# Kernel optimization log

Hardware: AMD Instinct MI355X
Metric: run time of the kernel (lower is better)

Reference implementation:

```python
import jax, jax.numpy as jnp
import numpy as np

B, S, E, H = 4, 2048, 2048, 16
D = E // H  # 128


def _rope(x, sin, cos):
    # x: (B, S, H, D); sin/cos: (S, D//2)
    x1, x2 = jnp.split(x, 2, axis=-1)
    c = cos[None, :, None, :]
    s = sin[None, :, None, :]
    return jnp.concatenate([x1 * c - x2 * s, x1 * s + x2 * c], axis=-1)


def setup_inputs() -> dict:
    key = jax.random.key(0)
    ks = jax.random.split(key, 12)
    inp = {
        "x_q": jax.random.normal(ks[0], (B, S, E), jnp.float32),
        "x_kv": jax.random.normal(ks[1], (B, S, E), jnp.float32),
        "Wq": jax.random.normal(ks[2], (E, E), jnp.float32) / np.sqrt(E),
        "bq": jnp.zeros((E,), jnp.float32),
        "Wk": jax.random.normal(ks[3], (E, E), jnp.float32) / np.sqrt(E),
        "bk": jnp.zeros((E,), jnp.float32),
        "Wv": jax.random.normal(ks[4], (E, E), jnp.float32) / np.sqrt(E),
        "bv": jnp.zeros((E,), jnp.float32),
        "Wo": jax.random.normal(ks[5], (E, E), jnp.float32) / np.sqrt(E),
        "bo": jnp.zeros((E,), jnp.float32),
        "angles": jax.random.uniform(ks[6], (2, S, D // 2), jnp.float32),
        "attn_mask": jnp.ones((B, S), jnp.int32),
        "causal": 0,
        "k_rope": 1,
    }
    return inp


def reference(x_q, x_kv, Wq, bq, Wk, bk, Wv, bv, Wo, bo, angles, attn_mask, causal, k_rope):
    sin, cos = angles[0], angles[1]
    q = (x_q @ Wq.T + bq).reshape(B, S, H, D)
    k = (x_kv @ Wk.T + bk).reshape(B, S, H, D)
    v = (x_kv @ Wv.T + bv).reshape(B, S, H, D)
    q = _rope(q, sin, cos)
    if k_rope:
        k = _rope(k, sin, cos)
    # scaled dot-product attention, heads leading: (B, H, S, S)
    scores = jnp.einsum("bqhd,bkhd->bhqk", q, k) / np.sqrt(D).astype(np.float32)
    mask = attn_mask.astype(bool)[:, None, None, :]  # (B,1,1,S_kv)
    if causal:
        cm = jnp.tril(jnp.ones((S, S), bool))[None, None]
        mask = mask & cm
    scores = jnp.where(mask, scores, jnp.finfo(scores.dtype).min)
    probs = jax.nn.softmax(scores, axis=-1)
    attn = jnp.einsum("bhqk,bkhd->bqhd", probs, v).reshape(B, S, E)
    return attn @ Wo.T + bo
```

## Files before the change

### kernel.cpp

```cpp
#include <hip/hip_runtime.h>
#include <hip/hip_bf16.h>


typedef __bf16 bf16;
typedef __bf16 bf16x8 __attribute__((ext_vector_type(8)));
typedef __bf16 bf16x4 __attribute__((ext_vector_type(4)));
typedef __bf16 bf16x2 __attribute__((ext_vector_type(2)));
typedef float  f32x4  __attribute__((ext_vector_type(4)));
typedef float  f32x16 __attribute__((ext_vector_type(16)));

constexpr int Bc = 4, Sc = 2048, Ec = 2048, Hc = 16, Dc = 128;
constexpr int Mc = Bc * Sc;

__device__ __forceinline__ void async16(const void* g, void* l) {
  __builtin_amdgcn_global_load_lds(
      (const __attribute__((address_space(1))) void*)g,
      (__attribute__((address_space(3))) void*)l, 16, 0, 0);
}

__device__ __forceinline__ unsigned int pkbf(float a, float b) {
  union { bf16x2 v; unsigned int u; } c;
  c.v[0] = (bf16)a; c.v[1] = (bf16)b;
  return c.u;
}

__device__ __forceinline__ int swzb32(int r, int kb) {
  int b = r * 64 + kb;
  return b ^ (((b >> 9) & 1) << 5);
}

__global__ void cvt_multi(const float* s0, const float* s1, const float* s2, const float* s3,
                          bf16* d0, bf16* d1, bf16* d2, bf16* d3, int n8) {
  const float* src; bf16* dst;
  switch (blockIdx.y) {
    case 0:  src = s0; dst = d0; break;
    case 1:  src = s1; dst = d1; break;
    case 2:  src = s2; dst = d2; break;
    default: src = s3; dst = d3; break;
  }
  int i = blockIdx.x * blockDim.x + threadIdx.x;
  const int stride = gridDim.x * blockDim.x;
  for (; i < n8; i += stride) {
    const float4 a = *((const float4*)src + (size_t)i * 2);
    const float4 b = *((const float4*)src + (size_t)i * 2 + 1);
    bf16x8 o;
    o[0] = (bf16)a.x; o[1] = (bf16)a.y; o[2] = (bf16)a.z; o[3] = (bf16)a.w;
    o[4] = (bf16)b.x; o[5] = (bf16)b.y; o[6] = (bf16)b.z; o[7] = (bf16)b.w;
    *(bf16x8*)(dst + (size_t)i * 8) = o;
  }
}

template <int OUT>
__global__ __launch_bounds__(512, 2) void gemm8(
    const bf16* __restrict__ A, const bf16* __restrict__ Bm,
    const float* __restrict__ bias, void* __restrict__ Cout, int Mblocks)
{
  __shared__ __align__(16) bf16 lds[4 * 16384];
  const int tid = threadIdx.x;
  const int w = tid >> 6, lane = tid & 63;
  const int l15 = lane & 15, l16 = lane >> 4;
  const int wm = w >> 2, wn = w & 3;
  const int id = blockIdx.x;
  const int nwg = Mblocks * 8, cpx = nwg >> 3;
  const int swz = (id & 7) * cpx + (id >> 3);
  const int by = swz >> 3, bx = swz & 7;
  const long m0 = (long)by * 256, n0 = (long)bx * 256;
  constexpr int NT = 64;

  auto stA = [&](int buf, long kt, int j) {
    int c = w * 128 + j * 64 + lane;
    int cs = c ^ (((c >> 5) & 1) << 1);
    async16(A + (m0 + (cs >> 2)) * 2048 + kt + (cs & 3) * 8,
            &lds[buf * 16384 + c * 8]);
  };
  auto stB = [&](int buf, long kt, int j) {
    int c = w * 128 + j * 64 + lane;
    int cs = c ^ (((c >> 5) & 1) << 1);
    async16(Bm + (n0 + (cs >> 2)) * 2048 + kt + (cs & 3) * 8,
            &lds[buf * 16384 + 8192 + c * 8]);
  };

  f32x4 acc[8][4];
#pragma unroll
  for (int a = 0; a < 8; ++a)
#pragma unroll
    for (int b = 0; b < 4; ++b) acc[a][b] = f32x4{0.f, 0.f, 0.f, 0.f};

  stA(0, 0, 0);  stA(0, 0, 1);  stB(0, 0, 0);  stB(0, 0, 1);
  stA(1, 32, 0); stA(1, 32, 1); stB(1, 32, 0); stB(1, 32, 1);
  stA(2, 64, 0); stA(2, 64, 1); stB(2, 64, 0); stB(2, 64, 1);
  asm volatile("s_waitcnt vmcnt(8)" ::: "memory");
  __builtin_amdgcn_s_barrier();

  int cur = 0, nx = 3;
  for (int t = 0; t < NT; ++t) {
    const char* Ab = (const char*)&lds[cur * 16384];
    const char* Bb = Ab + 16384;
    const long ktn = (long)(t + 3) * 32;
    const bool pf = (t < NT - 3);

    bf16x8 af[8], bf0[2];
#pragma unroll
    for (int mf = 0; mf < 8; ++mf)
      af[mf] = *(const bf16x8*)(Ab + swzb32(wm * 128 + mf * 16 + l15, l16 * 16));
#pragma unroll
    for (int nf = 0; nf < 2; ++nf)
      bf0[nf] = *(const bf16x8*)(Bb + swzb32(wn * 64 + nf * 16 + l15, l16 * 16));
    if (pf) { stA(nx, ktn, 0); stA(nx, ktn, 1); }
    asm volatile("" ::: "memory");
    __builtin_amdgcn_s_barrier();
    __builtin_amdgcn_s_setprio(1);
#pragma unroll
    for (int mf = 0; mf < 8; ++mf)
#pragma unroll
      for (int nf = 0; nf < 2; ++nf)
        acc[mf][nf] = __builtin_amdgcn_mfma_f32_16x16x32_bf16(af[mf], bf0[nf], acc[mf][nf], 0, 0, 0);
    __builtin_amdgcn_s_setprio(0);
    __builtin_amdgcn_s_barrier();

    bf16x8 bf1[2];
#pragma unroll
    for (int nf = 0; nf < 2; ++nf)
      bf1[nf] = *(const bf16x8*)(Bb + swzb32(wn * 64 + (2 + nf) * 16 + l15, l16 * 16));
    if (pf) { stB(nx, ktn, 0); stB(nx, ktn, 1); }
    asm volatile("" ::: "memory");
    __builtin_amdgcn_s_barrier();
    __builtin_amdgcn_s_setprio(1);
#pragma unroll
    for (int mf = 0; mf < 8; ++mf)
#pragma unroll
      for (int nf = 0; nf < 2; ++nf)
        acc[mf][2 + nf] = __builtin_amdgcn_mfma_f32_16x16x32_bf16(af[mf], bf1[nf], acc[mf][2 + nf], 0, 0, 0);
    __builtin_amdgcn_s_setprio(0);
    if (t < NT - 3)       { asm volatile("s_waitcnt vmcnt(8)" ::: "memory"); }
    else if (t == NT - 3) { asm volatile("s_waitcnt vmcnt(4)" ::: "memory"); }
    else if (t == NT - 2) { asm volatile("s_waitcnt vmcnt(0)" ::: "memory"); }
    __builtin_amdgcn_s_barrier();
    cur = (cur + 1) & 3;
    nx  = (nx + 1) & 3;
  }

#pragma unroll
  for (int mf = 0; mf < 8; ++mf)
#pragma unroll
    for (int nf = 0; nf < 4; ++nf) {
      const long m = m0 + wm * 128 + mf * 16 + l16 * 4;
      const long n = n0 + wn * 64 + nf * 16 + l15;
      const float bv = bias[n];
      if (OUT == 2) {
        const long bb = m >> 11, ss = m & 2047;
        const long head = n >> 7, d = n & 127;
        bf16x4 st;
#pragma unroll
        for (int i = 0; i < 4; ++i) st[i] = (bf16)(acc[mf][nf][i] + bv);
        *(bf16x4*)((bf16*)Cout + ((((bb << 4) + head) << 7) + d) * 2048 + ss) = st;
      } else {
#pragma unroll
        for (int i = 0; i < 4; ++i) {
          float v = acc[mf][nf][i] + bv;
          if (OUT == 1) ((bf16*)Cout)[(m + i) * 2048 + n] = (bf16)v;
          else          ((float*)Cout)[(m + i) * 2048 + n] = v;
        }
      }
    }
}

__global__ void rope_kernel(bf16* __restrict__ x, const float* __restrict__ angles,
                            const int* __restrict__ flag, int force)
{
  if (!force && flag[0] == 0) return;
  const int t = threadIdx.x;
  const long R = (long)blockIdx.x * 64 + (t >> 2);
  const int d0 = (t & 3) * 16;
  const long s = (R / Hc) % Sc;
  bf16* rowp = x + R * Dc;
  bf16x8 lo0 = *(bf16x8*)(rowp + d0);
  bf16x8 lo1 = *(bf16x8*)(rowp + d0 + 8);
  bf16x8 hi0 = *(bf16x8*)(rowp + d0 + 64);
  bf16x8 hi1 = *(bf16x8*)(rowp + d0 + 72);
  const float* sp = angles + s * 64 + d0;
  const float* cp = angles + 131072 + s * 64 + d0;
  bf16x8 a0, a1, b0, b1;
#pragma unroll
  for (int j = 0; j < 8; ++j) {
    float c = cp[j], sn = sp[j];
    float x1 = (float)lo0[j], x2 = (float)hi0[j];
    a0[j] = (bf16)(x1 * c - x2 * sn);
    b0[j] = (bf16)(x1 * sn + x2 * c);
    float c1 = cp[j + 8], sn1 = sp[j + 8];
    float y1 = (float)lo1[j], y2 = (float)hi1[j];
    a1[j] = (bf16)(y1 * c1 - y2 * sn1);
    b1[j] = (bf16)(y1 * sn1 + y2 * c1);
  }
  *(bf16x8*)(rowp + d0)      = a0;
  *(bf16x8*)(rowp + d0 + 8)  = a1;
  *(bf16x8*)(rowp + d0 + 64) = b0;
  *(bf16x8*)(rowp + d0 + 72) = b1;
}

__global__ __launch_bounds__(256, 2) void attn_kernel(
    const bf16* __restrict__ q0, const bf16* __restrict__ k0,
    const bf16* __restrict__ vt, const int* __restrict__ mask,
    const int* __restrict__ causal_p, const float* __restrict__ angles,
    bf16* __restrict__ attn_out)
{
  __shared__ __align__(16) bf16 Ks[2][64 * 128];
  __shared__ __align__(16) bf16 Vs[128 * 64];

  const int tid = threadIdx.x, wid = tid >> 6, lane = tid & 63;
  const int l31 = lane & 31, h = lane >> 5;
  const int id = blockIdx.x;
  const int swz = (id & 7) * 128 + (id >> 3);
  const int bh = swz >> 4, qb = swz & 15;
  const int b = bh >> 4, hh = bh & 15;
  const int q_glob = qb * 128 + wid * 32 + l31;
  const int causal_f = causal_p[0];
  const float SC = 0.08838834764831845f * 1.4426950408889634f;
  const float NEG = -3.0e38f;

  auto stageK = [&](int kv0s, int bufs) {
#pragma unroll
    for (int it = 0; it < 4; ++it) {
      int g = it * 256 + tid;
      int r = g >> 4, gp = g & 15;
      async16(k0 + ((size_t)(b * Sc + kv0s + r) * Hc + hh) * Dc + ((gp ^ (r & 15)) << 3),
              &Ks[bufs][g * 8]);
    }
  };
  auto stageV = [&](int kv0s) {
#pragma unroll
    for (int it = 0; it < 4; ++it) {
      int g = it * 256 + tid;
      int r = g >> 3, gp = g & 7;
      async16(vt + ((size_t)bh * Dc + r) * Sc + kv0s + ((gp ^ (r & 7)) << 3),
              &Vs[g * 8]);
    }
  };

  bf16x8 qf[8];
  {
    const bf16* qrow = q0 + ((size_t)(b * Sc + q_glob) * Hc + hh) * Dc;
#pragma unroll
    for (int dc = 0; dc < 4; ++dc) {
      bf16x8 lo = *(const bf16x8*)(qrow + dc * 16 + h * 8);
      bf16x8 hi = *(const bf16x8*)(qrow + (dc + 4) * 16 + h * 8);
      const float* sp = angles + (size_t)q_glob * 64 + dc * 16 + h * 8;
      union { float4 v[2]; float f[8]; } sn, cs;
      sn.v[0] = ((const float4*)sp)[0];
      sn.v[1] = ((const float4*)sp)[1];
      cs.v[0] = ((const float4*)(sp + 131072))[0];
      cs.v[1] = ((const float4*)(sp + 131072))[1];
#pragma unroll
      for (int j = 0; j < 8; ++j) {
        float x1 = (float)lo[j], x2 = (float)hi[j];
        qf[dc][j]     = (bf16)(SC * (x1 * cs.f[j] - x2 * sn.f[j]));
        qf[dc + 4][j] = (bf16)(SC * (x1 * sn.f[j] + x2 * cs.f[j]));
      }
    }
  }

  f32x16 o[4];
#pragma unroll
  for (int db = 0; db < 4; ++db)
#pragma unroll
    for (int r = 0; r < 16; ++r) o[db][r] = 0.f;
  float mrun = NEG, lrun = 0.f;

  stageK(0, 0);
  const int mv0 = mask[b * Sc + lane];
  asm volatile("s_waitcnt vmcnt(0)" ::: "memory");
  __builtin_amdgcn_s_barrier();
  unsigned long long mbits = __ballot(mv0 != 0);
  int cur = 0;

  for (int kv0 = 0; kv0 < Sc; kv0 += 64) {
    const int kvn = kv0 + 64;
    const bool has_next = (kvn < Sc);
    unsigned long long mbits_next = ~0ull;
    if (has_next) {
      const int mvn = mask[b * Sc + kvn + lane];
      mbits_next = __ballot(mvn != 0);
    }
    stageV(kv0);
    if (has_next) stageK(kvn, cur ^ 1);

    f32x16 s;
#pragma unroll
    for (int r = 0; r < 16; ++r) s[r] = 0.f;
    __builtin_amdgcn_s_setprio(1);
#pragma unroll
    for (int dc = 0; dc < 8; ++dc) {
      bf16x8 kf = *(const bf16x8*)&Ks[cur][l31 * 128 + (((dc * 2 + h) ^ (l31 & 15)) << 3)];
      s = __builtin_amdgcn_mfma_f32_32x32x16_bf16(kf, qf[dc], s, 0, 0, 0);
    }
    __builtin_amdgcn_s_setprio(0);
    if (mbits != ~0ull) {
#pragma unroll
      for (int r = 0; r < 16; ++r) {
        int off = (r & 3) + 8 * (r >> 2) + 4 * h;
        if (!((mbits >> off) & 1)) s[r] = NEG;
      }
    }
    if (causal_f) {
#pragma unroll
      for (int r = 0; r < 16; ++r) {
        int kvg = kv0 + (r & 3) + 8 * (r >> 2) + 4 * h;
        if (kvg > q_glob) s[r] = NEG;
      }
    }
    {
      float tmax = s[0];
#pragma unroll
      for (int r = 1; r < 16; ++r) tmax = fmaxf(tmax, s[r]);
      tmax = fmaxf(tmax, __shfl_xor(tmax, 32));
      if (!__all(tmax <= mrun + 8.0f)) {
        const float mnew = fmaxf(mrun, tmax);
        const float alpha = __builtin_amdgcn_exp2f(mrun - mnew);
#pragma unroll
        for (int db = 0; db < 4; ++db)
#pragma unroll
          for (int r = 0; r < 16; ++r) o[db][r] *= alpha;
        lrun *= alpha;
        mrun = mnew;
      }
      float rs = 0.f;
#pragma unroll
      for (int r = 0; r < 16; ++r) {
        s[r] = __builtin_amdgcn_exp2f(s[r] - mrun);
        rs += s[r];
      }
      rs += __shfl_xor(rs, 32);
      lrun += rs;
    }
    unsigned int dw0 = pkbf(s[0], s[1]),   dw1 = pkbf(s[2], s[3]);
    unsigned int dw2 = pkbf(s[4], s[5]),   dw3 = pkbf(s[6], s[7]);
    unsigned int dw4 = pkbf(s[8], s[9]),   dw5 = pkbf(s[10], s[11]);
    unsigned int dw6 = pkbf(s[12], s[13]), dw7 = pkbf(s[14], s[15]);
    asm volatile("v_permlane32_swap_b32 %0, %1" : "+v"(dw0), "+v"(dw2));
    asm volatile("v_permlane32_swap_b32 %0, %1" : "+v"(dw1), "+v"(dw3));
    asm volatile("v_permlane32_swap_b32 %0, %1" : "+v"(dw4), "+v"(dw6));
    asm volatile("v_permlane32_swap_b32 %0, %1" : "+v"(dw5), "+v"(dw7));
    union { unsigned int u[4]; bf16x8 v; } pf0, pf1;
    pf0.u[0] = dw0; pf0.u[1] = dw1; pf0.u[2] = dw2; pf0.u[3] = dw3;
    pf1.u[0] = dw4; pf1.u[1] = dw5; pf1.u[2] = dw6; pf1.u[3] = dw7;

    if (has_next) { asm volatile("s_waitcnt vmcnt(4)" ::: "memory"); }
    else          { asm volatile("s_waitcnt vmcnt(0)" ::: "memory"); }
    __builtin_amdgcn_s_barrier();

    __builtin_amdgcn_s_setprio(1);
#pragma unroll
    for (int ksb = 0; ksb < 2; ++ksb) {
      const bf16x8 pfv = ksb ? pf1.v : pf0.v;
#pragma unroll
      for (int db = 0; db < 4; ++db) {
        const int dr = db * 32 + l31;
        bf16x8 vb = *(const bf16x8*)&Vs[dr * 64 + (((ksb * 2 + h) ^ (dr & 7)) << 3)];
        o[db] = __builtin_amdgcn_mfma_f32_32x32x16_bf16(vb, pfv, o[db], 0, 0, 0);
      }
    }
    __builtin_amdgcn_s_setprio(0);

#pragma unroll
    for (int r = 0; r < 16; ++r) s[r] = 0.f;
    __builtin_amdgcn_s_setprio(1);
#pragma unroll
    for (int dc = 0; dc < 8; ++dc) {
      bf16x8 kf = *(const bf16x8*)&Ks[cur][(32 + l31) * 128 + (((dc * 2 + h) ^ (l31 & 15)) << 3)];
      s = __builtin_amdgcn_mfma_f32_32x32x16_bf16(kf, qf[dc], s, 0, 0, 0);
    }
    __builtin_amdgcn_s_setprio(0);
    if (mbits != ~0ull) {
#pragma unroll
      for (int r = 0; r < 16; ++r) {
        int off = 32 + (r & 3) + 8 * (r >> 2) + 4 * h;
        if (!((mbits >> off) & 1)) s[r] = NEG;
      }
    }
    if (causal_f) {
#pragma unroll
      for (int r = 0; r < 16; ++r) {
        int kvg = kv0 + 32 + (r & 3) + 8 * (r >> 2) + 4 * h;
        if (kvg > q_glob) s[r] = NEG;
      }
    }
    {
      float tmax = s[0];
#pragma unroll
      for (int r = 1; r < 16; ++r) tmax = fmaxf(tmax, s[r]);
      tmax = fmaxf(tmax, __shfl_xor(tmax, 32));
      if (!__all(tmax <= mrun + 8.0f)) {
        const float mnew = fmaxf(mrun, tmax);
        const float alpha = __builtin_amdgcn_exp2f(mrun - mnew);
#pragma unroll
        for (int db = 0; db < 4; ++db)
#pragma unroll
          for (int r = 0; r < 16; ++r) o[db][r] *= alpha;
        lrun *= alpha;
        mrun = mnew;
      }
      float rs = 0.f;
#pragma unroll
      for (int r = 0; r < 16; ++r) {
        s[r] = __builtin_amdgcn_exp2f(s[r] - mrun);
        rs += s[r];
      }
      rs += __shfl_xor(rs, 32);
      lrun += rs;
    }
    dw0 = pkbf(s[0], s[1]);   dw1 = pkbf(s[2], s[3]);
    dw2 = pkbf(s[4], s[5]);   dw3 = pkbf(s[6], s[7]);
    dw4 = pkbf(s[8], s[9]);   dw5 = pkbf(s[10], s[11]);
    dw6 = pkbf(s[12], s[13]); dw7 = pkbf(s[14], s[15]);
    asm volatile("v_permlane32_swap_b32 %0, %1" : "+v"(dw0), "+v"(dw2));
    asm volatile("v_permlane32_swap_b32 %0, %1" : "+v"(dw1), "+v"(dw3));
    asm volatile("v_permlane32_swap_b32 %0, %1" : "+v"(dw4), "+v"(dw6));
    asm volatile("v_permlane32_swap_b32 %0, %1" : "+v"(dw5), "+v"(dw7));
    pf0.u[0] = dw0; pf0.u[1] = dw1; pf0.u[2] = dw2; pf0.u[3] = dw3;
    pf1.u[0] = dw4; pf1.u[1] = dw5; pf1.u[2] = dw6; pf1.u[3] = dw7;

    __builtin_amdgcn_s_setprio(1);
#pragma unroll
    for (int ksb = 0; ksb < 2; ++ksb) {
      const bf16x8 pfv = ksb ? pf1.v : pf0.v;
#pragma unroll
      for (int db = 0; db < 4; ++db) {
        const int dr = db * 32 + l31;
        bf16x8 vb = *(const bf16x8*)&Vs[dr * 64 + ((((2 + ksb) * 2 + h) ^ (dr & 7)) << 3)];
        o[db] = __builtin_amdgcn_mfma_f32_32x32x16_bf16(vb, pfv, o[db], 0, 0, 0);
      }
    }
    __builtin_amdgcn_s_setprio(0);

    asm volatile("s_waitcnt vmcnt(0)" ::: "memory");
    __builtin_amdgcn_s_barrier();
    cur ^= 1;
    mbits = mbits_next;
  }

  const float inv = 1.0f / lrun;
  bf16* orow = attn_out + ((size_t)(b * Sc + q_glob) * Hc + hh) * Dc;
#pragma unroll
  for (int db = 0; db < 4; ++db)
#pragma unroll
    for (int rq = 0; rq < 4; ++rq) {
      bf16x4 st;
#pragma unroll
      for (int i = 0; i < 4; ++i) st[i] = (bf16)(o[db][rq * 4 + i] * inv);
      *(bf16x4*)(orow + db * 32 + rq * 8 + 4 * h) = st;
    }
}

extern "C" void kernel_launch(void* const* d_in, const int* in_sizes, int n_in,
                              void* d_out, int out_size, void* d_ws, size_t ws_size,
                              hipStream_t stream)
{
  const float* x_q    = (const float*)d_in[0];
  const float* x_kv   = (const float*)d_in[1];
  const float* Wq     = (const float*)d_in[2];
  const float* bq     = (const float*)d_in[3];
  const float* Wk     = (const float*)d_in[4];
  const float* bk     = (const float*)d_in[5];
  const float* Wv     = (const float*)d_in[6];
  const float* bv     = (const float*)d_in[7];
  const float* Wo     = (const float*)d_in[8];
  const float* bo     = (const float*)d_in[9];
  const float* angles = (const float*)d_in[10];
  const int*   amask  = (const int*)d_in[11];
  const int*   causal = (const int*)d_in[12];
  const int*   k_rope = (const int*)d_in[13];
  float* out = (float*)d_out;

  char* ws = (char*)d_ws;
  const size_t MB32 = (size_t)33554432;
  bf16* xq16  = (bf16*)(ws);
  bf16* xkv16 = (bf16*)(ws + MB32);
  bf16* wq16  = (bf16*)(ws + 2 * MB32);
  bf16* wk16  = wq16 + 4194304;
  bf16* wv16  = wk16 + 4194304;
  bf16* wo16  = wv16 + 4194304;
  bf16* q0    = (bf16*)(ws + 3 * MB32);
  bf16* k0    = (bf16*)(ws + 4 * MB32);
  bf16* Vt     = xq16;
  bf16* attn16 = xkv16;

  cvt_multi<<<dim3(1024, 2), 256, 0, stream>>>(x_q, x_kv, x_q, x_kv,
                                               xq16, xkv16, xq16, xkv16, Mc * Ec / 8);
  cvt_multi<<<dim3(256, 4), 256, 0, stream>>>(Wq, Wk, Wv, Wo,
                                              wq16, wk16, wv16, wo16, Ec * Ec / 8);

  const int gemmBlocks = (Mc / 256) * (Ec / 256);
  gemm8<1><<<gemmBlocks, 512, 0, stream>>>(xq16,  wq16, bq, q0, Mc / 256);
  gemm8<1><<<gemmBlocks, 512, 0, stream>>>(xkv16, wk16, bk, k0, Mc / 256);
  gemm8<2><<<gemmBlocks, 512, 0, stream>>>(xkv16, wv16, bv, Vt, Mc / 256);

  rope_kernel<<<2048, 256, 0, stream>>>(k0, angles, k_rope, 0);

  attn_kernel<<<1024, 256, 0, stream>>>(q0, k0, Vt, amask, causal, angles, attn16);

  gemm8<0><<<gemmBlocks, 512, 0, stream>>>(attn16, wo16, bo, out, Mc / 256);
}
```

Before: 513.3 us.

## Shrink GEMM M-tile to 128 with 3-stage pipeline; batch attention QK MFMAs

Result: slower. 538.1 us (+4.8%).

```diff
diff --git a/kernel.cpp b/kernel.cpp
--- a/kernel.cpp
+++ b/kernel.cpp
@@ -55,7 +55,7 @@
     const bf16* __restrict__ A, const bf16* __restrict__ Bm,
     const float* __restrict__ bias, void* __restrict__ Cout, int Mblocks)
 {
-  __shared__ __align__(16) bf16 lds[4 * 16384];
+  __shared__ __align__(16) bf16 lds[3 * 12288];
   const int tid = threadIdx.x;
   const int w = tid >> 6, lane = tid & 63;
   const int l15 = lane & 15, l16 = lane >> 4;
@@ -64,54 +64,53 @@
   const int nwg = Mblocks * 8, cpx = nwg >> 3;
   const int swz = (id & 7) * cpx + (id >> 3);
   const int by = swz >> 3, bx = swz & 7;
-  const long m0 = (long)by * 256, n0 = (long)bx * 256;
+  const long m0 = (long)by * 128, n0 = (long)bx * 256;
   constexpr int NT = 64;
 
-  auto stA = [&](int buf, long kt, int j) {
-    int c = w * 128 + j * 64 + lane;
+  auto stA = [&](int buf, long kt) {
+    int c = tid;
     int cs = c ^ (((c >> 5) & 1) << 1);
     async16(A + (m0 + (cs >> 2)) * 2048 + kt + (cs & 3) * 8,
-            &lds[buf * 16384 + c * 8]);
+            &lds[buf * 12288 + c * 8]);
   };
   auto stB = [&](int buf, long kt, int j) {
-    int c = w * 128 + j * 64 + lane;
+    int c = j * 512 + tid;
     int cs = c ^ (((c >> 5) & 1) << 1);
     async16(Bm + (n0 + (cs >> 2)) * 2048 + kt + (cs & 3) * 8,
-            &lds[buf * 16384 + 8192 + c * 8]);
+            &lds[buf * 12288 + 4096 + c * 8]);
   };
 
-  f32x4 acc[8][4];
-#pragma unroll
-  for (int a = 0; a < 8; ++a)
+  f32x4 acc[4][4];
+#pragma unroll
+  for (int a = 0; a < 4; ++a)
 #pragma unroll
     for (int b = 0; b < 4; ++b) acc[a][b] = f32x4{0.f, 0.f, 0.f, 0.f};
 
-  stA(0, 0, 0);  stA(0, 0, 1);  stB(0, 0, 0);  stB(0, 0, 1);
-  stA(1, 32, 0); stA(1, 32, 1); stB(1, 32, 0); stB(1, 32, 1);
-  stA(2, 64, 0); stA(2, 64, 1); stB(2, 64, 0); stB(2, 64, 1);
-  asm volatile("s_waitcnt vmcnt(8)" ::: "memory");
+  stA(0, 0);  stB(0, 0, 0);  stB(0, 0, 1);
+  stA(1, 32); stB(1, 32, 0); stB(1, 32, 1);
+  asm volatile("s_waitcnt vmcnt(3)" ::: "memory");
   __builtin_amdgcn_s_barrier();
 
-  int cur = 0, nx = 3;
+  int cur = 0, nx = 2;
   for (int t = 0; t < NT; ++t) {
-    const char* Ab = (const char*)&lds[cur * 16384];
-    const char* Bb = Ab + 16384;
-    const long ktn = (long)(t + 3) * 32;
-    const bool pf = (t < NT - 3);
-
-    bf16x8 af[8], bf0[2];
-#pragma unroll
-    for (int mf = 0; mf < 8; ++mf)
-      af[mf] = *(const bf16x8*)(Ab + swzb32(wm * 128 + mf * 16 + l15, l16 * 16));
+    const char* Ab = (const char*)&lds[cur * 12288];
+    const char* Bb = Ab + 8192;
+    const long ktn = (long)(t + 2) * 32;
+    const bool pf = (t < NT - 2);
+
+    bf16x8 af[4], bf0[2];
+#pragma unroll
+    for (int mf = 0; mf < 4; ++mf)
+      af[mf] = *(const bf16x8*)(Ab + swzb32(wm * 64 + mf * 16 + l15, l16 * 16));
 #pragma unroll
     for (int nf = 0; nf < 2; ++nf)
       bf0[nf] = *(const bf16x8*)(Bb + swzb32(wn * 64 + nf * 16 + l15, l16 * 16));
-    if (pf) { stA(nx, ktn, 0); stA(nx, ktn, 1); }
+    if (pf) stA(nx, ktn);
     asm volatile("" ::: "memory");
     __builtin_amdgcn_s_barrier();
     __builtin_amdgcn_s_setprio(1);
 #pragma unroll
-    for (int mf = 0; mf < 8; ++mf)
+    for (int mf = 0; mf < 4; ++mf)
 #pragma unroll
       for (int nf = 0; nf < 2; ++nf)
         acc[mf][nf] = __builtin_amdgcn_mfma_f32_16x16x32_bf16(af[mf], bf0[nf], acc[mf][nf], 0, 0, 0);
@@ -127,24 +126,23 @@
     __builtin_amdgcn_s_barrier();
     __builtin_amdgcn_s_setprio(1);
 #pragma unroll
-    for (int mf = 0; mf < 8; ++mf)
+    for (int mf = 0; mf < 4; ++mf)
 #pragma unroll
       for (int nf = 0; nf < 2; ++nf)
         acc[mf][2 + nf] = __builtin_amdgcn_mfma_f32_16x16x32_bf16(af[mf], bf1[nf], acc[mf][2 + nf], 0, 0, 0);
     __builtin_amdgcn_s_setprio(0);
-    if (t < NT - 3)       { asm volatile("s_waitcnt vmcnt(8)" ::: "memory"); }
-    else if (t == NT - 3) { asm volatile("s_waitcnt vmcnt(4)" ::: "memory"); }
+    if (t < NT - 2)       { asm volatile("s_waitcnt vmcnt(3)" ::: "memory"); }
     else if (t == NT - 2) { asm volatile("s_waitcnt vmcnt(0)" ::: "memory"); }
     __builtin_amdgcn_s_barrier();
-    cur = (cur + 1) & 3;
-    nx  = (nx + 1) & 3;
+    cur = (cur == 2) ? 0 : cur + 1;
+    nx  = (nx  == 2) ? 0 : nx  + 1;
   }
 
 #pragma unroll
-  for (int mf = 0; mf < 8; ++mf)
+  for (int mf = 0; mf < 4; ++mf)
 #pragma unroll
     for (int nf = 0; nf < 4; ++nf) {
-      const long m = m0 + wm * 128 + mf * 16 + l16 * 4;
+      const long m = m0 + wm * 64 + mf * 16 + l16 * 4;
       const long n = n0 + wn * 64 + nf * 16 + l15;
       const float bv = bias[n];
       if (OUT == 2) {
@@ -284,34 +282,43 @@
     stageV(kv0);
     if (has_next) stageK(kvn, cur ^ 1);
 
-    f32x16 s;
-#pragma unroll
-    for (int r = 0; r < 16; ++r) s[r] = 0.f;
+    f32x16 s0, s1;
+#pragma unroll
+    for (int r = 0; r < 16; ++r) { s0[r] = 0.f; s1[r] = 0.f; }
     __builtin_amdgcn_s_setprio(1);
 #pragma unroll
     for (int dc = 0; dc < 8; ++dc) {
       bf16x8 kf = *(const bf16x8*)&Ks[cur][l31 * 128 + (((dc * 2 + h) ^ (l31 & 15)) << 3)];
-      s = __builtin_amdgcn_mfma_f32_32x32x16_bf16(kf, qf[dc], s, 0, 0, 0);
+      s0 = __builtin_amdgcn_mfma_f32_32x32x16_bf16(kf, qf[dc], s0, 0, 0, 0);
+    }
+#pragma unroll
+    for (int dc = 0; dc < 8; ++dc) {
+      bf16x8 kf = *(const bf16x8*)&Ks[cur][(32 + l31) * 128 + (((dc * 2 + h) ^ (l31 & 15)) << 3)];
+      s1 = __builtin_amdgcn_mfma_f32_32x32x16_bf16(kf, qf[dc], s1, 0, 0, 0);
     }
     __builtin_amdgcn_s_setprio(0);
+
     if (mbits != ~0ull) {
 #pragma unroll
       for (int r = 0; r < 16; ++r) {
         int off = (r & 3) + 8 * (r >> 2) + 4 * h;
-        if (!((mbits >> off) & 1)) s[r] = NEG;
+        if (!((mbits >> off) & 1)) s0[r] = NEG;
       }
     }
     if (causal_f) {
 #pragma unroll
       for (int r = 0; r < 16; ++r) {
         int kvg = kv0 + (r & 3) + 8 * (r >> 2) + 4 * h;
-        if (kvg > q_glob) s[r] = NEG;
+        if (kvg > q_glob) s0[r] = NEG;
       }
     }
     {
-      float tmax = s[0];
-#pragma unroll
-      for (int r = 1; r < 16; ++r) tmax = fmaxf(tmax, s[r]);
+      float t0 = fmaxf(s0[0], s0[1]),  t1 = fmaxf(s0[2], s0[3]);
+      float t2 = fmaxf(s0[4], s0[5]),  t3 = fmaxf(s0[6], s0[7]);
+      float t4 = fmaxf(s0[8], s0[9]),  t5 = fmaxf(s0[10], s0[11]);
+      float t6 = fmaxf(s0[12], s0[13]), t7 = fmaxf(s0[14], s0[15]);
+      t0 = fmaxf(t0, t1); t2 = fmaxf(t2, t3); t4 = fmaxf(t4, t5); t6 = fmaxf(t6, t7);
+      float tmax = fmaxf(fmaxf(t0, t2), fmaxf(t4, t6));
       tmax = fmaxf(tmax, __shfl_xor(tmax, 32));
       if (!__all(tmax <= mrun + 8.0f)) {
         const float mnew = fmaxf(mrun, tmax);
@@ -323,19 +330,21 @@
         lrun *= alpha;
         mrun = mnew;
       }
-      float rs = 0.f;
-#pragma unroll
-      for (int r = 0; r < 16; ++r) {
-        s[r] = __builtin_amdgcn_exp2f(s[r] - mrun);
-        rs += s[r];
-      }
+#pragma unroll
+      for (int r = 0; r < 16; ++r) s0[r] = __builtin_amdgcn_exp2f(s0[r] - mrun);
+      float u0 = s0[0] + s0[1],  u1 = s0[2] + s0[3];
+      float u2 = s0[4] + s0[5],  u3 = s0[6] + s0[7];
+      float u4 = s0[8] + s0[9],  u5 = s0[10] + s0[11];
+      float u6 = s0[12] + s0[13], u7 = s0[14] + s0[15];
+      u0 += u1; u2 += u3; u4 += u5; u6 += u7;
+      float rs = (u0 + u2) + (u4 + u6);
       rs += __shfl_xor(rs, 32);
       lrun += rs;
     }
-    unsigned int dw0 = pkbf(s[0], s[1]),   dw1 = pkbf(s[2], s[3]);
-    unsigned int dw2 = pkbf(s[4], s[5]),   dw3 = pkbf(s[6], s[7]);
-    unsigned int dw4 = pkbf(s[8], s[9]),   dw5 = pkbf(s[10], s[11]);
-    unsigned int dw6 = pkbf(s[12], s[13]), dw7 = pkbf(s[14], s[15]);
+    unsigned int dw0 = pkbf(s0[0], s0[1]),   dw1 = pkbf(s0[2], s0[3]);
+    unsigned int dw2 = pkbf(s0[4], s0[5]),   dw3 = pkbf(s0[6], s0[7]);
+    unsigned int dw4 = pkbf(s0[8], s0[9]),   dw5 = pkbf(s0[10], s0[11]);
+    unsigned int dw6 = pkbf(s0[12], s0[13]), dw7 = pkbf(s0[14], s0[15]);
     asm volatile("v_permlane32_swap_b32 %0, %1" : "+v"(dw0), "+v"(dw2));
     asm volatile("v_permlane32_swap_b32 %0, %1" : "+v"(dw1), "+v"(dw3));
     asm volatile("v_permlane32_swap_b32 %0, %1" : "+v"(dw4), "+v"(dw6));
@@ -361,33 +370,27 @@
     }
     __builtin_amdgcn_s_setprio(0);
 
-#pragma unroll
-    for (int r = 0; r < 16; ++r) s[r] = 0.f;
-    __builtin_amdgcn_s_setprio(1);
-#pragma unroll
-    for (int dc = 0; dc < 8; ++dc) {
-      bf16x8 kf = *(const bf16x8*)&Ks[cur][(32 + l31) * 128 + (((dc * 2 + h) ^ (l31 & 15)) << 3)];
-      s = __builtin_amdgcn_mfma_f32_32x32x16_bf16(kf, qf[dc], s, 0, 0, 0);
-    }
-    __builtin_amdgcn_s_setprio(0);
     if (mbits != ~0ull) {
 #pragma unroll
       for (int r = 0; r < 16; ++r) {
         int off = 32 + (r & 3) + 8 * (r >> 2) + 4 * h;
-        if (!((mbits >> off) & 1)) s[r] = NEG;
+        if (!((mbits >> off) & 1)) s1[r] = NEG;
       }
     }
     if (causal_f) {
 #pragma unroll
       for (int r = 0; r < 16; ++r) {
         int kvg = kv0 + 32 + (r & 3) + 8 * (r >> 2) + 4 * h;
-        if (kvg > q_glob) s[r] = NEG;
+        if (kvg > q_glob) s1[r] = NEG;
       }
     }
     {
-      float tmax = s[0];
-#pragma unroll
-      for (int r = 1; r < 16; ++r) tmax = fmaxf(tmax, s[r]);
+      float t0 = fmaxf(s1[0], s1[1]),  t1 = fmaxf(s1[2], s1[3]);
+      float t2 = fmaxf(s1[4], s1[5]),  t3 = fmaxf(s1[6], s1[7]);
+      float t4 = fmaxf(s1[8], s1[9]),  t5 = fmaxf(s1[10], s1[11]);
+      float t6 = fmaxf(s1[12], s1[13]), t7 = fmaxf(s1[14], s1[15]);
+      t0 = fmaxf(t0, t1); t2 = fmaxf(t2, t3); t4 = fmaxf(t4, t5); t6 = fmaxf(t6, t7);
+      float tmax = fmaxf(fmaxf(t0, t2), fmaxf(t4, t6));
       tmax = fmaxf(tmax, __shfl_xor(tmax, 32));
       if (!__all(tmax <= mrun + 8.0f)) {
         const float mnew = fmaxf(mrun, tmax);
@@ -399,19 +402,21 @@
         lrun *= alpha;
         mrun = mnew;
       }
-      float rs = 0.f;
-#pragma unroll
-      for (int r = 0; r < 16; ++r) {
-        s[r] = __builtin_amdgcn_exp2f(s[r] - mrun);
-        rs += s[r];
-      }
+#pragma unroll
+      for (int r = 0; r < 16; ++r) s1[r] = __builtin_amdgcn_exp2f(s1[r] - mrun);
+      float u0 = s1[0] + s1[1],  u1 = s1[2] + s1[3];
+      float u2 = s1[4] + s1[5],  u3 = s1[6] + s1[7];
+      float u4 = s1[8] + s1[9],  u5 = s1[10] + s1[11];
+      float u6 = s1[12] + s1[13], u7 = s1[14] + s1[15];
+      u0 += u1; u2 += u3; u4 += u5; u6 += u7;
+      float rs = (u0 + u2) + (u4 + u6);
       rs += __shfl_xor(rs, 32);
       lrun += rs;
     }
-    dw0 = pkbf(s[0], s[1]);   dw1 = pkbf(s[2], s[3]);
-    dw2 = pkbf(s[4], s[5]);   dw3 = pkbf(s[6], s[7]);
-    dw4 = pkbf(s[8], s[9]);   dw5 = pkbf(s[10], s[11]);
-    dw6 = pkbf(s[12], s[13]); dw7 = pkbf(s[14], s[15]);
+    dw0 = pkbf(s1[0], s1[1]);   dw1 = pkbf(s1[2], s1[3]);
+    dw2 = pkbf(s1[4], s1[5]);   dw3 = pkbf(s1[6], s1[7]);
+    dw4 = pkbf(s1[8], s1[9]);   dw5 = pkbf(s1[10], s1[11]);
+    dw6 = pkbf(s1[12], s1[13]); dw7 = pkbf(s1[14], s1[15]);
     asm volatile("v_permlane32_swap_b32 %0, %1" : "+v"(dw0), "+v"(dw2));
     asm volatile("v_permlane32_swap_b32 %0, %1" : "+v"(dw1), "+v"(dw3));
     asm volatile("v_permlane32_swap_b32 %0, %1" : "+v"(dw4), "+v"(dw6));
@@ -489,14 +494,14 @@
   cvt_multi<<<dim3(256, 4), 256, 0, stream>>>(Wq, Wk, Wv, Wo,
                                               wq16, wk16, wv16, wo16, Ec * Ec / 8);
 
-  const int gemmBlocks = (Mc / 256) * (Ec / 256);
-  gemm8<1><<<gemmBlocks, 512, 0, stream>>>(xq16,  wq16, bq, q0, Mc / 256);
-  gemm8<1><<<gemmBlocks, 512, 0, stream>>>(xkv16, wk16, bk, k0, Mc / 256);
-  gemm8<2><<<gemmBlocks, 512, 0, stream>>>(xkv16, wv16, bv, Vt, Mc / 256);
+  const int gemmBlocks = (Mc / 128) * (Ec / 256);
+  gemm8<1><<<gemmBlocks, 512, 0, stream>>>(xq16,  wq16, bq, q0, Mc / 128);
+  gemm8<1><<<gemmBlocks, 512, 0, stream>>>(xkv16, wk16, bk, k0, Mc / 128);
+  gemm8<2><<<gemmBlocks, 512, 0, stream>>>(xkv16, wv16, bv, Vt, Mc / 128);
 
   rope_kernel<<<2048, 256, 0, stream>>>(k0, angles, k_rope, 0);
 
   attn_kernel<<<1024, 256, 0, stream>>>(q0, k0, Vt, amask, causal, angles, attn16);
 
-  gemm8<0><<<gemmBlocks, 512, 0, stream>>>(attn16, wo16, bo, out, Mc / 256);
-}
+  gemm8<0><<<gemmBlocks, 512, 0, stream>>>(attn16, wo16, bo, out, Mc / 128);
+}
```

## Restructure GEMM to double-buffered 64-wide K tiles with four-phase quadrant schedule

Applied to the files above, without the earlier changes.

New measurement: 475.7 us. 7.3% less time.

```diff
diff --git a/kernel.cpp b/kernel.cpp
--- a/kernel.cpp
+++ b/kernel.cpp
@@ -22,11 +22,6 @@
   union { bf16x2 v; unsigned int u; } c;
   c.v[0] = (bf16)a; c.v[1] = (bf16)b;
   return c.u;
-}
-
-__device__ __forceinline__ int swzb32(int r, int kb) {
-  int b = r * 64 + kb;
-  return b ^ (((b >> 9) & 1) << 5);
 }
 
 __global__ void cvt_multi(const float* s0, const float* s1, const float* s2, const float* s3,
@@ -55,7 +50,7 @@
     const bf16* __restrict__ A, const bf16* __restrict__ Bm,
     const float* __restrict__ bias, void* __restrict__ Cout, int Mblocks)
 {
-  __shared__ __align__(16) bf16 lds[4 * 16384];
+  __shared__ __align__(16) bf16 lds[2 * 32768];
   const int tid = threadIdx.x;
   const int w = tid >> 6, lane = tid & 63;
   const int l15 = lane & 15, l16 = lane >> 4;
@@ -65,19 +60,19 @@
   const int swz = (id & 7) * cpx + (id >> 3);
   const int by = swz >> 3, bx = swz & 7;
   const long m0 = (long)by * 256, n0 = (long)bx * 256;
-  constexpr int NT = 64;
-
-  auto stA = [&](int buf, long kt, int j) {
-    int c = w * 128 + j * 64 + lane;
-    int cs = c ^ (((c >> 5) & 1) << 1);
-    async16(A + (m0 + (cs >> 2)) * 2048 + kt + (cs & 3) * 8,
-            &lds[buf * 16384 + c * 8]);
+  constexpr int NT = 32;
+
+  auto stA = [&](int buf, long kt, int p, int j) {
+    int ca = p + 2 * j;
+    int row = ca * 64 + (tid >> 3);
+    async16(A + (m0 + row) * 2048 + kt + (((tid & 7) ^ (row & 7)) << 3),
+            &lds[buf * 32768 + ca * 4096 + tid * 8]);
   };
-  auto stB = [&](int buf, long kt, int j) {
-    int c = w * 128 + j * 64 + lane;
-    int cs = c ^ (((c >> 5) & 1) << 1);
-    async16(Bm + (n0 + (cs >> 2)) * 2048 + kt + (cs & 3) * 8,
-            &lds[buf * 16384 + 8192 + c * 8]);
+  auto stB = [&](int buf, long kt, int p, int j) {
+    int cb = p + 4 * j + 2 * (tid >> 8);
+    int row = cb * 32 + ((tid & 255) >> 3);
+    async16(Bm + (n0 + row) * 2048 + kt + (((tid & 7) ^ (row & 7)) << 3),
+            &lds[buf * 32768 + 16384 + (p + 4 * j) * 2048 + (tid >> 8) * 4096 + (tid & 255) * 8]);
   };
 
   f32x4 acc[8][4];
@@ -86,66 +81,112 @@
 #pragma unroll
     for (int b = 0; b < 4; ++b) acc[a][b] = f32x4{0.f, 0.f, 0.f, 0.f};
 
-  stA(0, 0, 0);  stA(0, 0, 1);  stB(0, 0, 0);  stB(0, 0, 1);
-  stA(1, 32, 0); stA(1, 32, 1); stB(1, 32, 0); stB(1, 32, 1);
-  stA(2, 64, 0); stA(2, 64, 1); stB(2, 64, 0); stB(2, 64, 1);
-  asm volatile("s_waitcnt vmcnt(8)" ::: "memory");
+  stA(0, 0, 0, 0); stA(0, 0, 0, 1);
+  stB(0, 0, 0, 0); stB(0, 0, 0, 1);
+  stB(0, 0, 1, 0); stB(0, 0, 1, 1);
+  stA(0, 0, 1, 0); stA(0, 0, 1, 1);
+  asm volatile("s_waitcnt vmcnt(4)" ::: "memory");
   __builtin_amdgcn_s_barrier();
 
-  int cur = 0, nx = 3;
   for (int t = 0; t < NT; ++t) {
-    const char* Ab = (const char*)&lds[cur * 16384];
-    const char* Bb = Ab + 16384;
-    const long ktn = (long)(t + 3) * 32;
-    const bool pf = (t < NT - 3);
-
-    bf16x8 af[8], bf0[2];
-#pragma unroll
-    for (int mf = 0; mf < 8; ++mf)
-      af[mf] = *(const bf16x8*)(Ab + swzb32(wm * 128 + mf * 16 + l15, l16 * 16));
+    const int buf = t & 1, nbuf = buf ^ 1;
+    const int base = buf * 32768;
+    const long ktn = (long)(t + 1) * 64;
+    const bool pf = (t < NT - 1);
+    bf16x8 fa[4][2], fb0[2][2], fb1[2][2];
+
+#pragma unroll
+    for (int mf = 0; mf < 4; ++mf)
+#pragma unroll
+      for (int ks = 0; ks < 2; ++ks) {
+        int row = wm * 128 + mf * 16 + l15;
+        fa[mf][ks] = *(const bf16x8*)&lds[base + row * 64 + (((ks * 4 + l16) ^ (row & 7)) << 3)];
+      }
 #pragma unroll
     for (int nf = 0; nf < 2; ++nf)
-      bf0[nf] = *(const bf16x8*)(Bb + swzb32(wn * 64 + nf * 16 + l15, l16 * 16));
-    if (pf) { stA(nx, ktn, 0); stA(nx, ktn, 1); }
+#pragma unroll
+      for (int ks = 0; ks < 2; ++ks) {
+        int row = wn * 64 + nf * 16 + l15;
+        fb0[nf][ks] = *(const bf16x8*)&lds[base + 16384 + row * 64 + (((ks * 4 + l16) ^ (row & 7)) << 3)];
+      }
+    asm volatile("s_waitcnt vmcnt(2)" ::: "memory");
     asm volatile("" ::: "memory");
     __builtin_amdgcn_s_barrier();
     __builtin_amdgcn_s_setprio(1);
 #pragma unroll
-    for (int mf = 0; mf < 8; ++mf)
+    for (int mf = 0; mf < 4; ++mf)
 #pragma unroll
       for (int nf = 0; nf < 2; ++nf)
-        acc[mf][nf] = __builtin_amdgcn_mfma_f32_16x16x32_bf16(af[mf], bf0[nf], acc[mf][nf], 0, 0, 0);
-    __builtin_amdgcn_s_setprio(0);
-    __builtin_amdgcn_s_barrier();
-
-    bf16x8 bf1[2];
+#pragma unroll
+        for (int ks = 0; ks < 2; ++ks)
+          acc[mf][nf] = __builtin_amdgcn_mfma_f32_16x16x32_bf16(fa[mf][ks], fb0[nf][ks], acc[mf][nf], 0, 0, 0);
+    __builtin_amdgcn_s_setprio(0);
+
 #pragma unroll
     for (int nf = 0; nf < 2; ++nf)
-      bf1[nf] = *(const bf16x8*)(Bb + swzb32(wn * 64 + (2 + nf) * 16 + l15, l16 * 16));
-    if (pf) { stB(nx, ktn, 0); stB(nx, ktn, 1); }
+#pragma unroll
+      for (int ks = 0; ks < 2; ++ks) {
+        int row = wn * 64 + 32 + nf * 16 + l15;
+        fb1[nf][ks] = *(const bf16x8*)&lds[base + 16384 + row * 64 + (((ks * 4 + l16) ^ (row & 7)) << 3)];
+      }
+    if (pf) { stA(nbuf, ktn, 0, 0); stA(nbuf, ktn, 0, 1); stB(nbuf, ktn, 0, 0); stB(nbuf, ktn, 0, 1); }
+    if (pf) { asm volatile("s_waitcnt vmcnt(4)" ::: "memory"); }
+    else    { asm volatile("s_waitcnt vmcnt(0)" ::: "memory"); }
     asm volatile("" ::: "memory");
     __builtin_amdgcn_s_barrier();
     __builtin_amdgcn_s_setprio(1);
 #pragma unroll
-    for (int mf = 0; mf < 8; ++mf)
+    for (int mf = 0; mf < 4; ++mf)
 #pragma unroll
       for (int nf = 0; nf < 2; ++nf)
-        acc[mf][2 + nf] = __builtin_amdgcn_mfma_f32_16x16x32_bf16(af[mf], bf1[nf], acc[mf][2 + nf], 0, 0, 0);
-    __builtin_amdgcn_s_setprio(0);
-    if (t < NT - 3)       { asm volatile("s_waitcnt vmcnt(8)" ::: "memory"); }
-    else if (t == NT - 3) { asm volatile("s_waitcnt vmcnt(4)" ::: "memory"); }
-    else if (t == NT - 2) { asm volatile("s_waitcnt vmcnt(0)" ::: "memory"); }
+#pragma unroll
+        for (int ks = 0; ks < 2; ++ks)
+          acc[mf][2 + nf] = __builtin_amdgcn_mfma_f32_16x16x32_bf16(fa[mf][ks], fb1[nf][ks], acc[mf][2 + nf], 0, 0, 0);
+    __builtin_amdgcn_s_setprio(0);
+
+#pragma unroll
+    for (int mf = 0; mf < 4; ++mf)
+#pragma unroll
+      for (int ks = 0; ks < 2; ++ks) {
+        int row = wm * 128 + 64 + mf * 16 + l15;
+        fa[mf][ks] = *(const bf16x8*)&lds[base + row * 64 + (((ks * 4 + l16) ^ (row & 7)) << 3)];
+      }
+    if (pf) { stB(nbuf, ktn, 1, 0); stB(nbuf, ktn, 1, 1); }
+    asm volatile("" ::: "memory");
     __builtin_amdgcn_s_barrier();
-    cur = (cur + 1) & 3;
-    nx  = (nx + 1) & 3;
+    __builtin_amdgcn_s_setprio(1);
+#pragma unroll
+    for (int mf = 0; mf < 4; ++mf)
+#pragma unroll
+      for (int nf = 0; nf < 2; ++nf)
+#pragma unroll
+        for (int ks = 0; ks < 2; ++ks)
+          acc[4 + mf][nf] = __builtin_amdgcn_mfma_f32_16x16x32_bf16(fa[mf][ks], fb0[nf][ks], acc[4 + mf][nf], 0, 0, 0);
+    __builtin_amdgcn_s_setprio(0);
+
+    if (pf) {
+      stA(nbuf, ktn, 1, 0); stA(nbuf, ktn, 1, 1);
+      asm volatile("s_waitcnt vmcnt(4)" ::: "memory");
+    }
+    asm volatile("" ::: "memory");
+    __builtin_amdgcn_s_barrier();
+    __builtin_amdgcn_s_setprio(1);
+#pragma unroll
+    for (int mf = 0; mf < 4; ++mf)
+#pragma unroll
+      for (int nf = 0; nf < 2; ++nf)
+#pragma unroll
+        for (int ks = 0; ks < 2; ++ks)
+          acc[4 + mf][2 + nf] = __builtin_amdgcn_mfma_f32_16x16x32_bf16(fa[mf][ks], fb1[nf][ks], acc[4 + mf][2 + nf], 0, 0, 0);
+    __builtin_amdgcn_s_setprio(0);
   }
 
 #pragma unroll
   for (int mf = 0; mf < 8; ++mf)
 #pragma unroll
     for (int nf = 0; nf < 4; ++nf) {
-      const long m = m0 + wm * 128 + mf * 16 + l16 * 4;
-      const long n = n0 + wn * 64 + nf * 16 + l15;
+      const long m = m0 + wm * 128 + ((mf >> 2) * 64) + (mf & 3) * 16 + l16 * 4;
+      const long n = n0 + wn * 64 + ((nf >> 1) * 32) + (nf & 1) * 16 + l15;
       const float bv = bias[n];
       if (OUT == 2) {
         const long bb = m >> 11, ss = m & 2047;
```
